# Kernel tuning notes

Measured on AMD Instinct MI355X. Metric: run time of the kernel, lower is better.

Reference implementation:

```python
import jax, jax.numpy as jnp
import numpy as np

N_NODE = 1_000_000
N_BOND = 100_000
K_TWIST = 40
MAX_ORDER = 8
N_DOMAIN = 10_000
SIGMA_MAX = float(np.pi)  # config.sigma_max (=1) * pi


def setup_inputs() -> dict:
    key = jax.random.key(0)
    k1, k2, k3, k4, k5 = jax.random.split(key, 5)
    pos = jax.random.normal(k1, (N_NODE, 3), jnp.float32) * 10.0
    info_level = jax.random.uniform(k2, (N_BOND,), jnp.float32)
    # bond annotation: [order, u, v]
    uv = jax.random.randint(k3, (N_BOND, 2), 0, N_NODE, dtype=jnp.int32)
    order = (jnp.arange(N_BOND, dtype=jnp.int32) % MAX_ORDER)
    tor_bonds_anno = jnp.concatenate([order[:, None], uv], axis=1)
    # twisted nodes: bond b (order b%MAX_ORDER, group g=b//MAX_ORDER) twists
    # nodes g*K_TWIST .. g*K_TWIST+K_TWIST-1  -> disjoint within each order level
    b = jnp.arange(N_BOND, dtype=jnp.int32)
    nodes = (b // MAX_ORDER)[:, None] * K_TWIST + jnp.arange(K_TWIST, dtype=jnp.int32)[None, :]
    index_tor = jnp.repeat(b, K_TWIST)
    twisted_nodes_anno = jnp.stack([index_tor, nodes.reshape(-1)], axis=1)
    # rigid domains: contiguous blocks of nodes
    node_index = jnp.arange(N_NODE, dtype=jnp.int32)
    domain_index = node_index // (N_NODE // N_DOMAIN)
    eps = jax.random.normal(k4, (N_BOND,), jnp.float32)
    uniform_angles = jax.random.uniform(k5, (N_BOND,), jnp.float32, minval=-np.pi, maxval=np.pi)
    return {
        "pos": pos, "info_level": info_level,
        "tor_bonds_anno": tor_bonds_anno, "twisted_nodes_anno": twisted_nodes_anno,
        "domain_index": domain_index, "node_index": node_index,
        "eps": eps, "uniform_angles": uniform_angles, "from_prior": 1,
    }


def _rodrigues(axis, angle):
    # axis: [B,3] unit vectors, angle: [B] -> R: [B,3,3]
    c = jnp.cos(angle)[:, None, None]
    s = jnp.sin(angle)[:, None, None]
    ax, ay, az = axis[:, 0], axis[:, 1], axis[:, 2]
    zero = jnp.zeros_like(ax)
    K = jnp.stack([
        jnp.stack([zero, -az, ay], -1),
        jnp.stack([az, zero, -ax], -1),
        jnp.stack([-ay, ax, zero], -1),
    ], axis=1)  # [B,3,3]
    aaT = axis[:, :, None] * axis[:, None, :]
    I = jnp.eye(3, dtype=axis.dtype)[None]
    return c * I + s * K + (1.0 - c) * aaT


def _torsion_and_kabsch(pos, info_level, eps, uniform_angles,
                        tor_bonds_anno, twisted_nodes_anno,
                        domain_index, node_index, from_prior):
    tor_order = tor_bonds_anno[:, 0]
    u, v = tor_bonds_anno[:, 1], tor_bonds_anno[:, 2]
    index_tor = twisted_nodes_anno[:, 0]
    tnodes = twisted_nodes_anno[:, 1]

    sigmas = (1.0 - info_level) * SIGMA_MAX
    angles_wn = eps * sigmas  # wrapped-normal sample (rotation is 2pi-periodic)
    if from_prior:
        angles = jnp.where(info_level == 0, uniform_angles, angles_wn)
    else:
        angles = angles_wn

    pos_tor = pos
    # sequential application by torsion order (axes move as parents rotate)
    for o in range(MAX_ORDER):
        axis_raw = pos_tor[v] - pos_tor[u]
        axis = axis_raw / (jnp.linalg.norm(axis_raw, axis=-1, keepdims=True) + 1e-12)
        R = _rodrigues(axis, angles)                      # [n_bond,3,3]
        pivot = pos_tor[v]                                # rotate about atom v on the axis
        p = pos_tor[tnodes] - pivot[index_tor]            # [n_twisted,3]
        rot = jnp.einsum('nij,nj->ni', R[index_tor], p) + pivot[index_tor]
        mask = (tor_order[index_tor] == o)[:, None]
        delta = jnp.where(mask, rot - pos_tor[tnodes], 0.0)
        pos_tor = pos_tor.at[tnodes].add(delta)

    # decouple: per-domain Kabsch alignment of pos_tor back onto pos
    P = pos_tor[node_index]
    Q = pos[node_index]
    cnt = jax.ops.segment_sum(jnp.ones((P.shape[0],), P.dtype), domain_index, N_DOMAIN)[:, None]
    cP = jax.ops.segment_sum(P, domain_index, N_DOMAIN) / cnt
    cQ = jax.ops.segment_sum(Q, domain_index, N_DOMAIN) / cnt
    Pc = P - cP[domain_index]
    Qc = Q - cQ[domain_index]
    H = jax.ops.segment_sum(Pc[:, :, None] * Qc[:, None, :], domain_index, N_DOMAIN)  # [D,3,3]
    Uh, S, Vt = jnp.linalg.svd(H)
    V = jnp.swapaxes(Vt, 1, 2)
    d = jnp.sign(jnp.linalg.det(jnp.matmul(V, jnp.swapaxes(Uh, 1, 2))))  # [D]
    Vm = jnp.concatenate([V[:, :, :2], V[:, :, 2:] * d[:, None, None]], axis=2)
    Rg = jnp.matmul(Vm, jnp.swapaxes(Uh, 1, 2))            # [D,3,3], Rg @ p ~ q
    tg = cQ - jnp.einsum('dij,dj->di', Rg, cP)             # [D,3]
    corrected = jnp.einsum('nij,nj->ni', Rg[domain_index], P) + tg[domain_index]
    return pos_tor.at[node_index].set(corrected)


def reference(pos, info_level, tor_bonds_anno, twisted_nodes_anno,
              domain_index, node_index, eps, uniform_angles, from_prior):
    return _torsion_and_kabsch(pos, info_level, eps, uniform_angles,
                               tor_bonds_anno, twisted_nodes_anno,
                               domain_index, node_index, from_prior)
```

## Files before the change

kernel.cpp:

```cpp
#include <hip/hip_runtime.h>
#include <math.h>

#define N_NODE    1000000
#define N_BOND    100000
#define K_TWIST   40
#define MAX_ORDER 8
#define N_DOMAIN  10000
#define N_PER_DOM 100
#define N_GROUP   12500
#define N_TWIST   500000
#define SIGMA_MAXF 3.14159265358979323846f


#define WS_RT    0
#define WS_M0    120000
#define WS_M1    270000
#define WS_SUMS  420000
#define WS_PREP  570000
#define WS_FLOATS_NEEDED 1770000u


__global__ __launch_bounds__(256) void prep_k(
    const float* __restrict__ pos, const float* __restrict__ info_level,
    const int* __restrict__ anno, const float* __restrict__ eps,
    const float* __restrict__ uni, const int* __restrict__ from_prior_p,
    float* __restrict__ prep)
{
    int b = blockIdx.x * 256 + threadIdx.x;
    if (b >= N_BOND) return;
    int ord = anno[3*b];
    int u   = anno[3*b + 1];
    int v   = anno[3*b + 2];
    float info = info_level[b];
    float ang  = eps[b] * (1.0f - info) * SIGMA_MAXF;
    if (from_prior_p[0] != 0 && info == 0.0f) ang = uni[b];
    int o = b % MAX_ORDER;
    int g = b / MAX_ORDER;
    float* pr = prep + (size_t)(o * N_GROUP + g) * 12;
    pr[0] = cosf(ang);
    pr[1] = sinf(ang);
    pr[2] = pos[3*u+0]; pr[3] = pos[3*u+1]; pr[4] = pos[3*u+2];
    pr[5] = pos[3*v+0]; pr[6] = pos[3*v+1]; pr[7] = pos[3*v+2];
    int gu = (u < N_TWIST) ? (u / K_TWIST) : -1;
    int gv = (v < N_TWIST) ? (v / K_TWIST) : -1;
    ((int*)pr)[8]  = gu;
    ((int*)pr)[9]  = gv;
    ((int*)pr)[10] = (ord == o) ? 1 : 0;
    pr[11] = 0.f;
}

__global__ __launch_bounds__(256) void compose_k(
    const float* __restrict__ prep,
    const float* __restrict__ Mp, float* __restrict__ Mc, int o)
{
    int g = blockIdx.x * 256 + threadIdx.x;
    if (g >= N_GROUP) return;
    const float4* pr4 = (const float4*)(prep + (size_t)(o * N_GROUP + g) * 12);
    float4 f0 = pr4[0], f1 = pr4[1], f2 = pr4[2];
    float c = f0.x, s = f0.y;
    float pu0 = f0.z, pu1 = f0.w, pu2 = f1.x;
    float pv0 = f1.y, pv1 = f1.z, pv2 = f1.w;
    int gu = __float_as_int(f2.x);
    int gv = __float_as_int(f2.y);
    int ok = __float_as_int(f2.z);
    float* mg = Mc + 12 * g;
    if (!ok) {
        if (o == 0) {
            mg[0]=1.f; mg[1]=0.f; mg[2]=0.f;
            mg[3]=0.f; mg[4]=1.f; mg[5]=0.f;
            mg[6]=0.f; mg[7]=0.f; mg[8]=1.f;
            mg[9]=0.f; mg[10]=0.f; mg[11]=0.f;
        } else {
            const float* mp = Mp + 12 * g;
            #pragma unroll
            for (int k = 0; k < 12; k++) mg[k] = mp[k];
        }
        return;
    }
    if (o > 0) {
        if (gu >= 0) {
            const float* m = Mp + 12 * gu;
            float a = m[0]*pu0 + m[1]*pu1 + m[2]*pu2 + m[9];
            float b = m[3]*pu0 + m[4]*pu1 + m[5]*pu2 + m[10];
            float e = m[6]*pu0 + m[7]*pu1 + m[8]*pu2 + m[11];
            pu0 = a; pu1 = b; pu2 = e;
        }
        if (gv >= 0) {
            const float* m = Mp + 12 * gv;
            float a = m[0]*pv0 + m[1]*pv1 + m[2]*pv2 + m[9];
            float b = m[3]*pv0 + m[4]*pv1 + m[5]*pv2 + m[10];
            float e = m[6]*pv0 + m[7]*pv1 + m[8]*pv2 + m[11];
            pv0 = a; pv1 = b; pv2 = e;
        }
    }
    float ax = pv0-pu0, ay = pv1-pu1, az = pv2-pu2;
    float inv = 1.0f / (sqrtf(ax*ax + ay*ay + az*az) + 1e-12f);
    ax *= inv; ay *= inv; az *= inv;
    float t = 1.0f - c;
    float R00 = c + t*ax*ax,     R01 = -s*az + t*ax*ay, R02 =  s*ay + t*ax*az;
    float R10 =  s*az + t*ay*ax, R11 = c + t*ay*ay,     R12 = -s*ax + t*ay*az;
    float R20 = -s*ay + t*az*ax, R21 =  s*ax + t*az*ay, R22 = c + t*az*az;
    if (o == 0) {
        mg[0]=R00; mg[1]=R01; mg[2]=R02;
        mg[3]=R10; mg[4]=R11; mg[5]=R12;
        mg[6]=R20; mg[7]=R21; mg[8]=R22;
        mg[9]  = pv0 - (R00*pv0 + R01*pv1 + R02*pv2);
        mg[10] = pv1 - (R10*pv0 + R11*pv1 + R12*pv2);
        mg[11] = pv2 - (R20*pv0 + R21*pv1 + R22*pv2);
    } else {
        const float* mp = Mp + 12 * g;
        mg[0] = R00*mp[0] + R01*mp[3] + R02*mp[6];
        mg[1] = R00*mp[1] + R01*mp[4] + R02*mp[7];
        mg[2] = R00*mp[2] + R01*mp[5] + R02*mp[8];
        mg[3] = R10*mp[0] + R11*mp[3] + R12*mp[6];
        mg[4] = R10*mp[1] + R11*mp[4] + R12*mp[7];
        mg[5] = R10*mp[2] + R11*mp[5] + R12*mp[8];
        mg[6] = R20*mp[0] + R21*mp[3] + R22*mp[6];
        mg[7] = R20*mp[1] + R21*mp[4] + R22*mp[7];
        mg[8] = R20*mp[2] + R21*mp[5] + R22*mp[8];
        float d0 = mp[9]-pv0, d1 = mp[10]-pv1, d2 = mp[11]-pv2;
        mg[9]  = R00*d0 + R01*d1 + R02*d2 + pv0;
        mg[10] = R10*d0 + R11*d1 + R12*d2 + pv1;
        mg[11] = R20*d0 + R21*d1 + R22*d2 + pv2;
    }
}

__global__ void apply_k(const float* __restrict__ pos,
                        const float* __restrict__ Mf,
                        const float* __restrict__ rt,
                        float* __restrict__ out)
{
    int n = blockIdx.x * 256 + threadIdx.x;
    if (n >= N_NODE) return;
    const float* w = rt + 12 * (n / N_PER_DOM);
    float q0 = pos[3*n+0], q1 = pos[3*n+1], q2 = pos[3*n+2];
    float p0 = q0, p1 = q1, p2 = q2;
    if (n < N_TWIST) {
        const float* m = Mf + 12 * (n / K_TWIST);
        p0 = m[0]*q0 + m[1]*q1 + m[2]*q2 + m[9];
        p1 = m[3]*q0 + m[4]*q1 + m[5]*q2 + m[10];
        p2 = m[6]*q0 + m[7]*q1 + m[8]*q2 + m[11];
    }
    out[3*n+0] = w[0]*p0 + w[1]*p1 + w[2]*p2 + w[9];
    out[3*n+1] = w[3]*p0 + w[4]*p1 + w[5]*p2 + w[10];
    out[3*n+2] = w[6]*p0 + w[7]*p1 + w[8]*p2 + w[11];
}


__global__ __launch_bounds__(256) void compose_legacy_k(
    const float* __restrict__ pos, const float* __restrict__ info_level,
    const int* __restrict__ anno, const float* __restrict__ eps,
    const float* __restrict__ uni, const int* __restrict__ from_prior_p,
    const float* __restrict__ Mp, float* __restrict__ Mc, int o)
{
    int g = blockIdx.x * 256 + threadIdx.x;
    if (g >= N_GROUP) return;
    int b = g * MAX_ORDER + o;
    float* mg = Mc + 12 * g;
    if (anno[3*b] != o) {
        if (o == 0) {
            mg[0]=1.f; mg[1]=0.f; mg[2]=0.f;
            mg[3]=0.f; mg[4]=1.f; mg[5]=0.f;
            mg[6]=0.f; mg[7]=0.f; mg[8]=1.f;
            mg[9]=0.f; mg[10]=0.f; mg[11]=0.f;
        } else {
            const float* mp = Mp + 12 * g;
            #pragma unroll
            for (int k = 0; k < 12; k++) mg[k] = mp[k];
        }
        return;
    }
    int u = anno[3*b + 1];
    int v = anno[3*b + 2];
    float pu0 = pos[3*u+0], pu1 = pos[3*u+1], pu2 = pos[3*u+2];
    float pv0 = pos[3*v+0], pv1 = pos[3*v+1], pv2 = pos[3*v+2];
    if (o > 0) {
        if (u < N_TWIST) {
            const float* m = Mp + 12 * (u / K_TWIST);
            float a = m[0]*pu0 + m[1]*pu1 + m[2]*pu2 + m[9];
            float c = m[3]*pu0 + m[4]*pu1 + m[5]*pu2 + m[10];
            float e = m[6]*pu0 + m[7]*pu1 + m[8]*pu2 + m[11];
            pu0 = a; pu1 = c; pu2 = e;
        }
        if (v < N_TWIST) {
            const float* m = Mp + 12 * (v / K_TWIST);
            float a = m[0]*pv0 + m[1]*pv1 + m[2]*pv2 + m[9];
            float c = m[3]*pv0 + m[4]*pv1 + m[5]*pv2 + m[10];
            float e = m[6]*pv0 + m[7]*pv1 + m[8]*pv2 + m[11];
            pv0 = a; pv1 = c; pv2 = e;
        }
    }
    float info = info_level[b];
    float ang  = eps[b] * (1.0f - info) * SIGMA_MAXF;
    if (from_prior_p[0] != 0 && info == 0.0f) ang = uni[b];
    float ax = pv0-pu0, ay = pv1-pu1, az = pv2-pu2;
    float inv = 1.0f / (sqrtf(ax*ax + ay*ay + az*az) + 1e-12f);
    ax *= inv; ay *= inv; az *= inv;
    float c = cosf(ang), s = sinf(ang), t = 1.0f - c;
    float R00 = c + t*ax*ax,     R01 = -s*az + t*ax*ay, R02 =  s*ay + t*ax*az;
    float R10 =  s*az + t*ay*ax, R11 = c + t*ay*ay,     R12 = -s*ax + t*ay*az;
    float R20 = -s*ay + t*az*ax, R21 =  s*ax + t*az*ay, R22 = c + t*az*az;
    if (o == 0) {
        mg[0]=R00; mg[1]=R01; mg[2]=R02;
        mg[3]=R10; mg[4]=R11; mg[5]=R12;
        mg[6]=R20; mg[7]=R21; mg[8]=R22;
        mg[9]  = pv0 - (R00*pv0 + R01*pv1 + R02*pv2);
        mg[10] = pv1 - (R10*pv0 + R11*pv1 + R12*pv2);
        mg[11] = pv2 - (R20*pv0 + R21*pv1 + R22*pv2);
    } else {
        const float* mp = Mp + 12 * g;
        mg[0] = R00*mp[0] + R01*mp[3] + R02*mp[6];
        mg[1] = R00*mp[1] + R01*mp[4] + R02*mp[7];
        mg[2] = R00*mp[2] + R01*mp[5] + R02*mp[8];
        mg[3] = R10*mp[0] + R11*mp[3] + R12*mp[6];
        mg[4] = R10*mp[1] + R11*mp[4] + R12*mp[7];
        mg[5] = R10*mp[2] + R11*mp[5] + R12*mp[8];
        mg[6] = R20*mp[0] + R21*mp[3] + R22*mp[6];
        mg[7] = R20*mp[1] + R21*mp[4] + R22*mp[7];
        mg[8] = R20*mp[2] + R21*mp[5] + R22*mp[8];
        float d0 = mp[9]-pv0, d1 = mp[10]-pv1, d2 = mp[11]-pv2;
        mg[9]  = R00*d0 + R01*d1 + R02*d2 + pv0;
        mg[10] = R10*d0 + R11*d1 + R12*d2 + pv1;
        mg[11] = R20*d0 + R21*d1 + R22*d2 + pv2;
    }
}

__global__ void apply_low_k(const float* __restrict__ pos,
                            const float* __restrict__ Mf,
                            const float* __restrict__ rt,
                            float* __restrict__ out)
{
    int n = blockIdx.x * 256 + threadIdx.x;
    if (n >= N_TWIST) return;
    const float* m = Mf + 12 * (n / K_TWIST);
    const float* w = rt + 12 * (n / N_PER_DOM);
    float q0 = pos[3*n+0], q1 = pos[3*n+1], q2 = pos[3*n+2];
    float p0 = m[0]*q0 + m[1]*q1 + m[2]*q2 + m[9];
    float p1 = m[3]*q0 + m[4]*q1 + m[5]*q2 + m[10];
    float p2 = m[6]*q0 + m[7]*q1 + m[8]*q2 + m[11];
    out[3*n+0] = w[0]*p0 + w[1]*p1 + w[2]*p2 + w[9];
    out[3*n+1] = w[3]*p0 + w[4]*p1 + w[5]*p2 + w[10];
    out[3*n+2] = w[6]*p0 + w[7]*p1 + w[8]*p2 + w[11];
}

__global__ void apply_high_k(const float* __restrict__ pos,
                             const float* __restrict__ rt,
                             float* __restrict__ out)
{
    int i = blockIdx.x * 256 + threadIdx.x;
    int n = N_TWIST + i;
    if (n >= N_NODE) return;
    const float* w = rt + 12 * (n / N_PER_DOM);
    float q0 = pos[3*n+0], q1 = pos[3*n+1], q2 = pos[3*n+2];
    out[3*n+0] = w[0]*q0 + w[1]*q1 + w[2]*q2 + w[9];
    out[3*n+1] = w[3]*q0 + w[4]*q1 + w[5]*q2 + w[10];
    out[3*n+2] = w[6]*q0 + w[7]*q1 + w[8]*q2 + w[11];
}


__global__ __launch_bounds__(256) void reduce_k(const float* __restrict__ pos,
                                                const float* __restrict__ Mf,
                                                float* __restrict__ sums)
{
    int wave = threadIdx.x >> 6;
    int lane = threadIdx.x & 63;
    int d = blockIdx.x * 4 + wave;
    float a[15];
    #pragma unroll
    for (int k = 0; k < 15; k++) a[k] = 0.f;
    for (int i = lane; i < N_PER_DOM; i += 64) {
        int n = d * N_PER_DOM + i;
        float q0 = pos[3*n+0], q1 = pos[3*n+1], q2 = pos[3*n+2];
        float p0 = q0, p1 = q1, p2 = q2;
        if (n < N_TWIST) {
            const float* m = Mf + 12 * (n / K_TWIST);
            p0 = m[0]*q0 + m[1]*q1 + m[2]*q2 + m[9];
            p1 = m[3]*q0 + m[4]*q1 + m[5]*q2 + m[10];
            p2 = m[6]*q0 + m[7]*q1 + m[8]*q2 + m[11];
        }
        a[0]+=p0;    a[1]+=p1;    a[2]+=p2;
        a[3]+=q0;    a[4]+=q1;    a[5]+=q2;
        a[6]+=p0*q0; a[7]+=p0*q1; a[8]+=p0*q2;
        a[9]+=p1*q0; a[10]+=p1*q1;a[11]+=p1*q2;
        a[12]+=p2*q0;a[13]+=p2*q1;a[14]+=p2*q2;
    }
    #pragma unroll
    for (int off = 32; off > 0; off >>= 1)
        #pragma unroll
        for (int k = 0; k < 15; k++) a[k] += __shfl_down(a[k], off);
    if (lane == 0) {
        float* sd = sums + (size_t)d * 15;
        #pragma unroll
        for (int k = 0; k < 15; k++) sd[k] = a[k];
    }
}

__device__ inline void cross3d(const double a[3], const double b[3], double r[3])
{
    r[0] = a[1]*b[2] - a[2]*b[1];
    r[1] = a[2]*b[0] - a[0]*b[2];
    r[2] = a[0]*b[1] - a[1]*b[0];
}

__device__ void kabsch_from_sums(const float* s, float* __restrict__ rt)
{
    const double inv_n = 1.0 / (double)N_PER_DOM;
    double sP[3] = { s[0], s[1], s[2] };
    double sQ[3] = { s[3], s[4], s[5] };
    double H[3][3];
    #pragma unroll
    for (int i = 0; i < 3; i++)
        #pragma unroll
        for (int j = 0; j < 3; j++)
            H[i][j] = (double)s[6 + 3*i + j] - sP[i]*sQ[j]*inv_n;
    double A[3][3];
    #pragma unroll
    for (int i = 0; i < 3; i++)
        #pragma unroll
        for (int j = 0; j < 3; j++)
            A[i][j] = H[0][i]*H[0][j] + H[1][i]*H[1][j] + H[2][i]*H[2][j];
    double V[3][3] = {{1,0,0},{0,1,0},{0,0,1}};
    for (int sweep = 0; sweep < 30; sweep++) {
        double off = A[0][1]*A[0][1] + A[0][2]*A[0][2] + A[1][2]*A[1][2];
        double n2  = A[0][0]*A[0][0] + A[1][1]*A[1][1] + A[2][2]*A[2][2];
        if (off <= 1e-28 * n2) break;
        for (int pp = 0; pp < 3; pp++) {
            int p = (pp == 2) ? 1 : 0;
            int q = (pp == 0) ? 1 : 2;
            double apq = A[p][q];
            if (apq == 0.0) continue;
            double tau = (A[q][q] - A[p][p]) / (2.0 * apq);
            double tj  = (tau >= 0.0 ? 1.0 : -1.0) / (fabs(tau) + sqrt(1.0 + tau*tau));
            double cj  = 1.0 / sqrt(1.0 + tj*tj);
            double sj  = tj * cj;
            int r = 3 - p - q;
            double app = A[p][p], aqq = A[q][q];
            A[p][p] = app - tj*apq;
            A[q][q] = aqq + tj*apq;
            A[p][q] = 0.0; A[q][p] = 0.0;
            double arp = A[r][p], arq = A[r][q];
            A[r][p] = cj*arp - sj*arq; A[p][r] = A[r][p];
            A[r][q] = sj*arp + cj*arq; A[q][r] = A[r][q];
            #pragma unroll
            for (int k = 0; k < 3; k++) {
                double vp = V[k][p], vq = V[k][q];
                V[k][p] = cj*vp - sj*vq;
                V[k][q] = sj*vp + cj*vq;
            }
        }
    }
    double wv[3] = { A[0][0], A[1][1], A[2][2] };
    int i0 = 0, i1 = 1, i2 = 2;
    if (wv[i0] < wv[i1]) { int t = i0; i0 = i1; i1 = t; }
    if (wv[i0] < wv[i2]) { int t = i0; i0 = i2; i2 = t; }
    if (wv[i1] < wv[i2]) { int t = i1; i1 = i2; i2 = t; }
    double v0[3] = { V[0][i0], V[1][i0], V[2][i0] };
    double v1[3] = { V[0][i1], V[1][i1], V[2][i1] };
    double v2[3] = { V[0][i2], V[1][i2], V[2][i2] };
    double s0 = sqrt(fmax(wv[i0], 0.0));
    double Rg[3][3];
    if (s0 < 1e-200) {
        Rg[0][0]=1; Rg[0][1]=0; Rg[0][2]=0;
        Rg[1][0]=0; Rg[1][1]=1; Rg[1][2]=0;
        Rg[2][0]=0; Rg[2][1]=0; Rg[2][2]=1;
    } else {
        double u0[3], u1[3], u2[3];
        #pragma unroll
        for (int i = 0; i < 3; i++)
            u0[i] = H[i][0]*v0[0] + H[i][1]*v0[1] + H[i][2]*v0[2];
        double n0 = sqrt(u0[0]*u0[0] + u0[1]*u0[1] + u0[2]*u0[2]);
        if (n0 > 0.0) { u0[0]/=n0; u0[1]/=n0; u0[2]/=n0; }
        else { u0[0]=1; u0[1]=0; u0[2]=0; }
        #pragma unroll
        for (int i = 0; i < 3; i++)
            u1[i] = H[i][0]*v1[0] + H[i][1]*v1[1] + H[i][2]*v1[2];
        double dp = u0[0]*u1[0] + u0[1]*u1[1] + u0[2]*u1[2];
        u1[0] -= dp*u0[0]; u1[1] -= dp*u0[1]; u1[2] -= dp*u0[2];
        double n1 = sqrt(u1[0]*u1[0] + u1[1]*u1[1] + u1[2]*u1[2]);
        if (n1 > 1e-12 * n0) { u1[0]/=n1; u1[1]/=n1; u1[2]/=n1; }
        else {
            double tv[3] = { (fabs(u0[0]) < 0.9) ? 1.0 : 0.0,
                             (fabs(u0[0]) < 0.9) ? 0.0 : 1.0, 0.0 };
            cross3d(u0, tv, u1);
            double nn = sqrt(u1[0]*u1[0] + u1[1]*u1[1] + u1[2]*u1[2]);
            u1[0]/=nn; u1[1]/=nn; u1[2]/=nn;
        }
        cross3d(u0, u1, u2);
        double c12[3]; cross3d(v1, v2, c12);
        double detV = v0[0]*c12[0] + v0[1]*c12[1] + v0[2]*c12[2];
        double dsg = (detV >= 0.0) ? 1.0 : -1.0;
        #pragma unroll
        for (int r = 0; r < 3; r++)
            #pragma unroll
            for (int c = 0; c < 3; c++)
                Rg[r][c] = v0[r]*u0[c] + v1[r]*u1[c] + dsg*v2[r]*u2[c];
    }
    double cP[3] = { sP[0]*inv_n, sP[1]*inv_n, sP[2]*inv_n };
    double cQ[3] = { sQ[0]*inv_n, sQ[1]*inv_n, sQ[2]*inv_n };
    #pragma unroll
    for (int i = 0; i < 3; i++) {
        rt[3*i+0] = (float)Rg[i][0];
        rt[3*i+1] = (float)Rg[i][1];
        rt[3*i+2] = (float)Rg[i][2];
        rt[9+i] = (float)(cQ[i] - (Rg[i][0]*cP[0] + Rg[i][1]*cP[1] + Rg[i][2]*cP[2]));
    }
}

__global__ __launch_bounds__(128) void svd_k(const float* __restrict__ sums,
                                             float* __restrict__ rt)
{
    int d = blockIdx.x * 128 + threadIdx.x;
    if (d >= N_DOMAIN) return;
    kabsch_from_sums(sums + (size_t)d * 15, rt + (size_t)d * 12);
}

extern "C" void kernel_launch(void* const* d_in, const int* in_sizes, int n_in,
                              void* d_out, int out_size, void* d_ws, size_t ws_size,
                              hipStream_t stream)
{
    const float* pos        = (const float*)d_in[0];
    const float* info_level = (const float*)d_in[1];
    const int*   anno       = (const int*)  d_in[2];
    const float* eps        = (const float*)d_in[6];
    const float* uni        = (const float*)d_in[7];
    const int*   from_prior = (const int*)  d_in[8];
    float* out = (float*)d_out;
    float* ws  = (float*)d_ws;

    if (ws_size >= (size_t)WS_FLOATS_NEEDED * sizeof(float)) {
        float* rt   = ws + WS_RT;
        float* M0   = ws + WS_M0;
        float* M1   = ws + WS_M1;
        float* sums = ws + WS_SUMS;
        float* prep = ws + WS_PREP;

        prep_k<<<(N_BOND + 255)/256, 256, 0, stream>>>(
            pos, info_level, anno, eps, uni, from_prior, prep);

        for (int o = 0; o < MAX_ORDER; o++) {
            const float* Mp = (o & 1) ? M0 : M1;
            float*       Mc = (o & 1) ? M1 : M0;
            compose_k<<<(N_GROUP + 255)/256, 256, 0, stream>>>(prep, Mp, Mc, o);
        }
        float* Mf = M1;

        reduce_k<<<N_DOMAIN / 4, 256, 0, stream>>>(pos, Mf, sums);
        svd_k<<<(N_DOMAIN + 127)/128, 128, 0, stream>>>(sums, rt);
        apply_k<<<(N_NODE + 255)/256, 256, 0, stream>>>(pos, Mf, rt, out);
    } else {
        float* rt   = ws;
        float* M0   = out + (size_t)3 * N_TWIST;
        float* M1   = M0 + 12 * N_GROUP;
        float* sums = M1 + 12 * N_GROUP;

        for (int o = 0; o < MAX_ORDER; o++) {
            const float* Mp = (o & 1) ? M0 : M1;
            float*       Mc = (o & 1) ? M1 : M0;
            compose_legacy_k<<<(N_GROUP + 255)/256, 256, 0, stream>>>(
                pos, info_level, anno, eps, uni, from_prior, Mp, Mc, o);
        }
        float* Mf = M1;

        reduce_k<<<N_DOMAIN / 4, 256, 0, stream>>>(pos, Mf, sums);
        svd_k<<<(N_DOMAIN + 127)/128, 128, 0, stream>>>(sums, rt);
        apply_low_k<<<(N_TWIST + 255)/256, 256, 0, stream>>>(pos, Mf, rt, out);
        apply_high_k<<<(N_NODE - N_TWIST + 255)/256, 256, 0, stream>>>(pos, rt, out);
    }
}
```

Before: 156.5 us.

## Fuse eight per-order compose launches into one persistent kernel with grid barriers

Result: slower. 244.1 us (+56.0%).

```diff
diff --git a/kernel.cpp b/kernel.cpp
--- a/kernel.cpp
+++ b/kernel.cpp
@@ -11,22 +11,39 @@
 #define N_TWIST   500000
 #define SIGMA_MAXF 3.14159265358979323846f
 
+#define CBLK  512
+#define CGRID ((N_GROUP + CBLK - 1) / CBLK)
+
 
 #define WS_RT    0
 #define WS_M0    120000
 #define WS_M1    270000
 #define WS_SUMS  420000
 #define WS_PREP  570000
-#define WS_FLOATS_NEEDED 1770000u
+#define WS_CTR   1770000
+#define WS_FLOATS_NEEDED 1770016u
+
+__device__ __forceinline__ float ld_coh(const float* p)
+{
+    return __hip_atomic_load(p, __ATOMIC_RELAXED, __HIP_MEMORY_SCOPE_AGENT);
+}
+__device__ __forceinline__ void st_coh(float* p, float v)
+{
+    __hip_atomic_store(p, v, __ATOMIC_RELAXED, __HIP_MEMORY_SCOPE_AGENT);
+}
 
 
 __global__ __launch_bounds__(256) void prep_k(
     const float* __restrict__ pos, const float* __restrict__ info_level,
     const int* __restrict__ anno, const float* __restrict__ eps,
     const float* __restrict__ uni, const int* __restrict__ from_prior_p,
-    float* __restrict__ prep)
+    float* __restrict__ prep, unsigned int* __restrict__ ctr)
 {
     int b = blockIdx.x * 256 + threadIdx.x;
+    if (b == 0) {
+        #pragma unroll
+        for (int k = 0; k < 8; k++) ctr[k] = 0u;
+    }
     if (b >= N_BOND) return;
     int ord = anno[3*b];
     int u   = anno[3*b + 1];
@@ -49,79 +66,116 @@
     pr[11] = 0.f;
 }
 
-__global__ __launch_bounds__(256) void compose_k(
+__global__ __launch_bounds__(CBLK) void chain_k(
     const float* __restrict__ prep,
-    const float* __restrict__ Mp, float* __restrict__ Mc, int o)
-{
-    int g = blockIdx.x * 256 + threadIdx.x;
-    if (g >= N_GROUP) return;
-    const float4* pr4 = (const float4*)(prep + (size_t)(o * N_GROUP + g) * 12);
-    float4 f0 = pr4[0], f1 = pr4[1], f2 = pr4[2];
-    float c = f0.x, s = f0.y;
-    float pu0 = f0.z, pu1 = f0.w, pu2 = f1.x;
-    float pv0 = f1.y, pv1 = f1.z, pv2 = f1.w;
-    int gu = __float_as_int(f2.x);
-    int gv = __float_as_int(f2.y);
-    int ok = __float_as_int(f2.z);
-    float* mg = Mc + 12 * g;
-    if (!ok) {
-        if (o == 0) {
-            mg[0]=1.f; mg[1]=0.f; mg[2]=0.f;
-            mg[3]=0.f; mg[4]=1.f; mg[5]=0.f;
-            mg[6]=0.f; mg[7]=0.f; mg[8]=1.f;
-            mg[9]=0.f; mg[10]=0.f; mg[11]=0.f;
-        } else {
-            const float* mp = Mp + 12 * g;
-            #pragma unroll
-            for (int k = 0; k < 12; k++) mg[k] = mp[k];
-        }
-        return;
-    }
-    if (o > 0) {
-        if (gu >= 0) {
-            const float* m = Mp + 12 * gu;
-            float a = m[0]*pu0 + m[1]*pu1 + m[2]*pu2 + m[9];
-            float b = m[3]*pu0 + m[4]*pu1 + m[5]*pu2 + m[10];
-            float e = m[6]*pu0 + m[7]*pu1 + m[8]*pu2 + m[11];
-            pu0 = a; pu1 = b; pu2 = e;
-        }
-        if (gv >= 0) {
-            const float* m = Mp + 12 * gv;
-            float a = m[0]*pv0 + m[1]*pv1 + m[2]*pv2 + m[9];
-            float b = m[3]*pv0 + m[4]*pv1 + m[5]*pv2 + m[10];
-            float e = m[6]*pv0 + m[7]*pv1 + m[8]*pv2 + m[11];
-            pv0 = a; pv1 = b; pv2 = e;
-        }
-    }
-    float ax = pv0-pu0, ay = pv1-pu1, az = pv2-pu2;
-    float inv = 1.0f / (sqrtf(ax*ax + ay*ay + az*az) + 1e-12f);
-    ax *= inv; ay *= inv; az *= inv;
-    float t = 1.0f - c;
-    float R00 = c + t*ax*ax,     R01 = -s*az + t*ax*ay, R02 =  s*ay + t*ax*az;
-    float R10 =  s*az + t*ay*ax, R11 = c + t*ay*ay,     R12 = -s*ax + t*ay*az;
-    float R20 = -s*ay + t*az*ax, R21 =  s*ax + t*az*ay, R22 = c + t*az*az;
-    if (o == 0) {
-        mg[0]=R00; mg[1]=R01; mg[2]=R02;
-        mg[3]=R10; mg[4]=R11; mg[5]=R12;
-        mg[6]=R20; mg[7]=R21; mg[8]=R22;
-        mg[9]  = pv0 - (R00*pv0 + R01*pv1 + R02*pv2);
-        mg[10] = pv1 - (R10*pv0 + R11*pv1 + R12*pv2);
-        mg[11] = pv2 - (R20*pv0 + R21*pv1 + R22*pv2);
-    } else {
-        const float* mp = Mp + 12 * g;
-        mg[0] = R00*mp[0] + R01*mp[3] + R02*mp[6];
-        mg[1] = R00*mp[1] + R01*mp[4] + R02*mp[7];
-        mg[2] = R00*mp[2] + R01*mp[5] + R02*mp[8];
-        mg[3] = R10*mp[0] + R11*mp[3] + R12*mp[6];
-        mg[4] = R10*mp[1] + R11*mp[4] + R12*mp[7];
-        mg[5] = R10*mp[2] + R11*mp[5] + R12*mp[8];
-        mg[6] = R20*mp[0] + R21*mp[3] + R22*mp[6];
-        mg[7] = R20*mp[1] + R21*mp[4] + R22*mp[7];
-        mg[8] = R20*mp[2] + R21*mp[5] + R22*mp[8];
-        float d0 = mp[9]-pv0, d1 = mp[10]-pv1, d2 = mp[11]-pv2;
-        mg[9]  = R00*d0 + R01*d1 + R02*d2 + pv0;
-        mg[10] = R10*d0 + R11*d1 + R12*d2 + pv1;
-        mg[11] = R20*d0 + R21*d1 + R22*d2 + pv2;
+    float* __restrict__ M0, float* __restrict__ M1,
+    unsigned int* __restrict__ ctr)
+{
+    int g = blockIdx.x * CBLK + threadIdx.x;
+    bool active = (g < N_GROUP);
+
+    #pragma unroll
+    for (int o = 0; o < MAX_ORDER; o++) {
+        float* Mp = (o & 1) ? M0 : M1;
+        float* Mc = (o & 1) ? M1 : M0;
+        if (active) {
+            const float4* pr4 =
+                (const float4*)(prep + (size_t)(o * N_GROUP + g) * 12);
+            float4 f0 = pr4[0], f1 = pr4[1], f2 = pr4[2];
+            float c = f0.x, s = f0.y;
+            float pu0 = f0.z, pu1 = f0.w, pu2 = f1.x;
+            float pv0 = f1.y, pv1 = f1.z, pv2 = f1.w;
+            int gu = __float_as_int(f2.x);
+            int gv = __float_as_int(f2.y);
+            int ok = __float_as_int(f2.z);
+            float* mg = Mc + 12 * g;
+            if (!ok) {
+                if (o == 0) {
+                    st_coh(mg+0,1.f); st_coh(mg+1,0.f); st_coh(mg+2,0.f);
+                    st_coh(mg+3,0.f); st_coh(mg+4,1.f); st_coh(mg+5,0.f);
+                    st_coh(mg+6,0.f); st_coh(mg+7,0.f); st_coh(mg+8,1.f);
+                    st_coh(mg+9,0.f); st_coh(mg+10,0.f); st_coh(mg+11,0.f);
+                } else {
+                    const float* mp = Mp + 12 * g;
+                    #pragma unroll
+                    for (int k = 0; k < 12; k++) st_coh(mg+k, ld_coh(mp+k));
+                }
+            } else {
+                if (o > 0) {
+                    if (gu >= 0) {
+                        const float* m = Mp + 12 * gu;
+                        float m0=ld_coh(m+0),m1=ld_coh(m+1),m2=ld_coh(m+2);
+                        float m3=ld_coh(m+3),m4=ld_coh(m+4),m5=ld_coh(m+5);
+                        float m6=ld_coh(m+6),m7=ld_coh(m+7),m8=ld_coh(m+8);
+                        float m9=ld_coh(m+9),mA=ld_coh(m+10),mB=ld_coh(m+11);
+                        float a = m0*pu0 + m1*pu1 + m2*pu2 + m9;
+                        float d = m3*pu0 + m4*pu1 + m5*pu2 + mA;
+                        float e = m6*pu0 + m7*pu1 + m8*pu2 + mB;
+                        pu0 = a; pu1 = d; pu2 = e;
+                    }
+                    if (gv >= 0) {
+                        const float* m = Mp + 12 * gv;
+                        float m0=ld_coh(m+0),m1=ld_coh(m+1),m2=ld_coh(m+2);
+                        float m3=ld_coh(m+3),m4=ld_coh(m+4),m5=ld_coh(m+5);
+                        float m6=ld_coh(m+6),m7=ld_coh(m+7),m8=ld_coh(m+8);
+                        float m9=ld_coh(m+9),mA=ld_coh(m+10),mB=ld_coh(m+11);
+                        float a = m0*pv0 + m1*pv1 + m2*pv2 + m9;
+                        float d = m3*pv0 + m4*pv1 + m5*pv2 + mA;
+                        float e = m6*pv0 + m7*pv1 + m8*pv2 + mB;
+                        pv0 = a; pv1 = d; pv2 = e;
+                    }
+                }
+                float ax = pv0-pu0, ay = pv1-pu1, az = pv2-pu2;
+                float inv = 1.0f / (sqrtf(ax*ax + ay*ay + az*az) + 1e-12f);
+                ax *= inv; ay *= inv; az *= inv;
+                float t = 1.0f - c;
+                float R00 = c + t*ax*ax,     R01 = -s*az + t*ax*ay, R02 =  s*ay + t*ax*az;
+                float R10 =  s*az + t*ay*ax, R11 = c + t*ay*ay,     R12 = -s*ax + t*ay*az;
+                float R20 = -s*ay + t*az*ax, R21 =  s*ax + t*az*ay, R22 = c + t*az*az;
+                if (o == 0) {
+                    st_coh(mg+0,R00); st_coh(mg+1,R01); st_coh(mg+2,R02);
+                    st_coh(mg+3,R10); st_coh(mg+4,R11); st_coh(mg+5,R12);
+                    st_coh(mg+6,R20); st_coh(mg+7,R21); st_coh(mg+8,R22);
+                    st_coh(mg+9,  pv0 - (R00*pv0 + R01*pv1 + R02*pv2));
+                    st_coh(mg+10, pv1 - (R10*pv0 + R11*pv1 + R12*pv2));
+                    st_coh(mg+11, pv2 - (R20*pv0 + R21*pv1 + R22*pv2));
+                } else {
+                    const float* mp = Mp + 12 * g;
+                    float m0=ld_coh(mp+0),m1=ld_coh(mp+1),m2=ld_coh(mp+2);
+                    float m3=ld_coh(mp+3),m4=ld_coh(mp+4),m5=ld_coh(mp+5);
+                    float m6=ld_coh(mp+6),m7=ld_coh(mp+7),m8=ld_coh(mp+8);
+                    float m9=ld_coh(mp+9),mA=ld_coh(mp+10),mB=ld_coh(mp+11);
+                    st_coh(mg+0, R00*m0 + R01*m3 + R02*m6);
+                    st_coh(mg+1, R00*m1 + R01*m4 + R02*m7);
+                    st_coh(mg+2, R00*m2 + R01*m5 + R02*m8);
+                    st_coh(mg+3, R10*m0 + R11*m3 + R12*m6);
+                    st_coh(mg+4, R10*m1 + R11*m4 + R12*m7);
+                    st_coh(mg+5, R10*m2 + R11*m5 + R12*m8);
+                    st_coh(mg+6, R20*m0 + R21*m3 + R22*m6);
+                    st_coh(mg+7, R20*m1 + R21*m4 + R22*m7);
+                    st_coh(mg+8, R20*m2 + R21*m5 + R22*m8);
+                    float d0 = m9-pv0, d1 = mA-pv1, d2 = mB-pv2;
+                    st_coh(mg+9,  R00*d0 + R01*d1 + R02*d2 + pv0);
+                    st_coh(mg+10, R10*d0 + R11*d1 + R12*d2 + pv1);
+                    st_coh(mg+11, R20*d0 + R21*d1 + R22*d2 + pv2);
+                }
+            }
+        }
+        if (o < MAX_ORDER - 1) {
+            __syncthreads();
+            if (threadIdx.x == 0) {
+                __hip_atomic_fetch_add(&ctr[o], 1u, __ATOMIC_RELAXED,
+                                       __HIP_MEMORY_SCOPE_AGENT);
+                long guard = 0;
+                while (__hip_atomic_load(&ctr[o], __ATOMIC_RELAXED,
+                                         __HIP_MEMORY_SCOPE_AGENT)
+                       < (unsigned)gridDim.x) {
+                    __builtin_amdgcn_s_sleep(4);
+                    if (++guard > (1L << 22)) break;
+                }
+            }
+            __syncthreads();
+        }
     }
 }
 
@@ -433,15 +487,12 @@
         float* M1   = ws + WS_M1;
         float* sums = ws + WS_SUMS;
         float* prep = ws + WS_PREP;
+        unsigned int* ctr = (unsigned int*)(ws + WS_CTR);
 
         prep_k<<<(N_BOND + 255)/256, 256, 0, stream>>>(
-            pos, info_level, anno, eps, uni, from_prior, prep);
-
-        for (int o = 0; o < MAX_ORDER; o++) {
-            const float* Mp = (o & 1) ? M0 : M1;
-            float*       Mc = (o & 1) ? M1 : M0;
-            compose_k<<<(N_GROUP + 255)/256, 256, 0, stream>>>(prep, Mp, Mc, o);
-        }
+            pos, info_level, anno, eps, uni, from_prior, prep, ctr);
+
+        chain_k<<<CGRID, CBLK, 0, stream>>>(prep, M0, M1, ctr);
         float* Mf = M1;
 
         reduce_k<<<N_DOMAIN / 4, 256, 0, stream>>>(pos, Mf, sums);
```
